# Performance work log

Hardware: AMD Instinct MI355X
Metric: run time of the kernel (lower is better)

## Reference

```python
import jax, jax.numpy as jnp
import numpy as np

N_NODES = 100000
N_EDGES = 3200000
D_IN = 256
D_OUT = 256


def setup_inputs() -> dict:
    key = jax.random.key(0)
    k1, k2, k3, k4, k5, k6 = jax.random.split(key, 6)
    x = jax.random.normal(k1, (N_NODES, D_IN), dtype=jnp.float32)
    edge_row = jax.random.randint(k2, (N_EDGES,), 0, N_NODES, dtype=jnp.int32)
    edge_col = jax.random.randint(k3, (N_EDGES,), 0, N_NODES, dtype=jnp.int32)
    edge_val = jax.random.uniform(k4, (N_EDGES,), dtype=jnp.float32)
    # nn.Linear params (PyTorch stores weight as [out, in]; we apply x @ W.T + b)
    bound = 1.0 / np.sqrt(D_IN)
    W = jax.random.uniform(k5, (D_OUT, D_IN), minval=-bound, maxval=bound, dtype=jnp.float32)
    b = jax.random.uniform(k6, (D_OUT,), minval=-bound, maxval=bound, dtype=jnp.float32)
    return {"x": x, "edge_row": edge_row, "edge_col": edge_col,
            "edge_val": edge_val, "W": W, "b": b}


def reference(x, edge_row, edge_col, edge_val, W, b):
    # SpMM: agg[i] = sum over edges e with row[e]==i of val[e] * x[col[e]]
    messages = edge_val[:, None] * x[edge_col]          # [E, D_in]
    agg = jax.ops.segment_sum(messages, edge_row, num_segments=N_NODES)  # [N, D_in]
    # Dense linear: agg @ W.T + b
    return jnp.einsum('nd,od->no', agg, W) + b
```

## Files before the change

### kernel.cpp

```cpp
#include <hip/hip_runtime.h>

#define THREADS 256

typedef __attribute__((ext_vector_type(8))) short short8;
typedef __attribute__((ext_vector_type(4))) float f32x4;

__device__ __forceinline__ unsigned short f2bf(float f) {
    unsigned u = __builtin_bit_cast(unsigned, f);
    return (unsigned short)((u + 0x7FFFu + ((u >> 16) & 1u)) >> 16);
}
__device__ __forceinline__ float bf2f_lo(unsigned u) { return __builtin_bit_cast(float, u << 16); }
__device__ __forceinline__ float bf2f_hi(unsigned u) { return __builtin_bit_cast(float, u & 0xFFFF0000u); }

#define P1B 1024

__global__ void fusedA_kernel(const int* __restrict__ row, const int* __restrict__ col,
                              const float* __restrict__ val, int* __restrict__ gcur,
                              uint2* __restrict__ estage,
                              const float* __restrict__ W, unsigned short* __restrict__ WbP,
                              const float4* __restrict__ x, uint4* __restrict__ xb,
                              int n_edges, int nbkt, int capB, int n8) {
    int b = blockIdx.x, tid = threadIdx.x;
    if (b < P1B) {
        __shared__ int h[512];
        __shared__ int curl[512];
        int E0 = (int)((long long)b * n_edges / P1B);
        int E1 = (int)((long long)(b + 1) * n_edges / P1B);
        for (int i = tid; i < 512; i += THREADS) h[i] = 0;
        __syncthreads();
        for (int e = E0 + tid; e < E1; e += THREADS)
            atomicAdd(&h[row[e] >> 8], 1);
        __syncthreads();
        for (int bk = tid; bk < nbkt; bk += THREADS) {
            int c = h[bk];
            curl[bk] = bk * capB + (c ? atomicAdd(&gcur[bk], c) : 0);
        }
        __syncthreads();
        for (int e = E0 + tid; e < E1; e += THREADS) {
            int r = row[e];
            int bk = r >> 8;
            int pos = atomicAdd(&curl[bk], 1);
            if (pos < (bk + 1) * capB)
                estage[pos] = make_uint2(((unsigned)(r & 255) << 24) | (unsigned)col[e],
                                         (unsigned)__float_as_int(val[e]));
        }
    } else if (b < P1B + 32) {
        int f = (b - P1B) * THREADS + tid;
        int l = f & 63, nt = (f >> 6) & 15, k0i = f >> 10;
        int r = nt * 16 + (l & 15);
        int koff = k0i * 32 + 8 * (l >> 4);
        const float4* s = reinterpret_cast<const float4*>(W + r * 256 + koff);
        float4 a = s[0], bb = s[1];
        uint4 o;
        o.x = (unsigned)f2bf(a.x) | ((unsigned)f2bf(a.y) << 16);
        o.y = (unsigned)f2bf(a.z) | ((unsigned)f2bf(a.w) << 16);
        o.z = (unsigned)f2bf(bb.x) | ((unsigned)f2bf(bb.y) << 16);
        o.w = (unsigned)f2bf(bb.z) | ((unsigned)f2bf(bb.w) << 16);
        reinterpret_cast<uint4*>(WbP)[f] = o;
    } else {
        int i = (b - P1B - 32) * THREADS + tid;
        if (i >= n8) return;
        float4 a = x[2 * i], bb = x[2 * i + 1];
        uint4 o;
        o.x = (unsigned)f2bf(a.x) | ((unsigned)f2bf(a.y) << 16);
        o.y = (unsigned)f2bf(a.z) | ((unsigned)f2bf(a.w) << 16);
        o.z = (unsigned)f2bf(bb.x) | ((unsigned)f2bf(bb.y) << 16);
        o.w = (unsigned)f2bf(bb.z) | ((unsigned)f2bf(bb.w) << 16);
        reinterpret_cast<uint4*>(xb)[i] = o;
    }
}

__global__ void p2_sort(const uint2* __restrict__ estage, const int* __restrict__ gcur,
                        int2* __restrict__ pr, int* __restrict__ offs,
                        int capB, int n_nodes, int nbkt) {
    __shared__ int red[256];
    __shared__ int h[256];
    __shared__ int curh[256];
    __shared__ int wsum[4];
    int b = blockIdx.x, tid = threadIdx.x;

    int partial = 0;
    for (int j = tid; j < b; j += THREADS) {
        int c = gcur[j];
        partial += c > capB ? capB : c;
    }
    red[tid] = partial;
    __syncthreads();
    #pragma unroll
    for (int s = 128; s > 0; s >>= 1) {
        if (tid < s) red[tid] += red[tid + s];
        __syncthreads();
    }
    int gb = red[0];
    int count = gcur[b]; if (count > capB) count = capB;
    int base = b * capB;

    h[tid] = 0;
    __syncthreads();
    for (int i = tid; i < count; i += THREADS)
        atomicAdd(&h[estage[base + i].x >> 24], 1);
    __syncthreads();
    int v = h[tid];
    int lane = tid & 63, w = tid >> 6;
    int incl = v;
    #pragma unroll
    for (int off = 1; off < 64; off <<= 1) {
        int t = __shfl_up(incl, off, 64);
        if (lane >= off) incl += t;
    }
    if (lane == 63) wsum[w] = incl;
    __syncthreads();
    int wo = 0;
    for (int i = 0; i < w; ++i) wo += wsum[i];
    int excl = wo + incl - v;
    int node = b * 256 + tid;
    if (node < n_nodes) offs[node] = gb + excl;
    curh[tid] = gb + excl;
    if (b == nbkt - 1 && tid == 0) offs[n_nodes] = gb + count;
    __syncthreads();
    for (int i = tid; i < count; i += THREADS) {
        uint2 p = estage[base + i];
        int q = atomicAdd(&curh[(int)(p.x >> 24)], 1);
        pr[q] = make_int2((int)(p.x & 0x00FFFFFFu), (int)p.y);
    }
}

template<int OUT_BF16>
__global__ void spmm_bf16_kernel(const uint2* __restrict__ xb, const int* __restrict__ offs,
                                 const int2* __restrict__ pr, void* __restrict__ outp,
                                 int nnodes) {
    int g = blockIdx.x & 7;
    int inst = blockIdx.x >> 3;
    int bkt = g + 8 * (inst >> 6);
    int wid = bkt * 256 + (inst & 63) * 4 + (threadIdx.x >> 6);
    int lane = threadIdx.x & 63;
    if (wid >= nnodes) return;
    int s = offs[wid], e = offs[wid + 1];
    float a0 = 0.f, a1 = 0.f, a2 = 0.f, a3 = 0.f;
    int i = s;
    if (i < e && (i & 1)) {
        int2 p = pr[i];
        uint2 xv = xb[(size_t)p.x * 64 + lane];
        float v = __int_as_float(p.y);
        a0 = fmaf(v, bf2f_lo(xv.x), a0); a1 = fmaf(v, bf2f_hi(xv.x), a1);
        a2 = fmaf(v, bf2f_lo(xv.y), a2); a3 = fmaf(v, bf2f_hi(xv.y), a3);
        ++i;
    }
    for (; i + 8 <= e; i += 8) {
        int4 pa = *reinterpret_cast<const int4*>(pr + i);
        int4 pb = *reinterpret_cast<const int4*>(pr + i + 2);
        int4 pc = *reinterpret_cast<const int4*>(pr + i + 4);
        int4 pd = *reinterpret_cast<const int4*>(pr + i + 6);
        uint2 x0 = xb[(size_t)pa.x * 64 + lane];
        uint2 x1 = xb[(size_t)pa.z * 64 + lane];
        uint2 x2 = xb[(size_t)pb.x * 64 + lane];
        uint2 x3 = xb[(size_t)pb.z * 64 + lane];
        uint2 x4_ = xb[(size_t)pc.x * 64 + lane];
        uint2 x5 = xb[(size_t)pc.z * 64 + lane];
        uint2 x6 = xb[(size_t)pd.x * 64 + lane];
        uint2 x7 = xb[(size_t)pd.z * 64 + lane];
        float v0 = __int_as_float(pa.y), v1 = __int_as_float(pa.w);
        float v2 = __int_as_float(pb.y), v3 = __int_as_float(pb.w);
        float v4 = __int_as_float(pc.y), v5 = __int_as_float(pc.w);
        float v6 = __int_as_float(pd.y), v7 = __int_as_float(pd.w);
        a0 = fmaf(v0, bf2f_lo(x0.x), a0); a1 = fmaf(v0, bf2f_hi(x0.x), a1);
        a2 = fmaf(v0, bf2f_lo(x0.y), a2); a3 = fmaf(v0, bf2f_hi(x0.y), a3);
        a0 = fmaf(v1, bf2f_lo(x1.x), a0); a1 = fmaf(v1, bf2f_hi(x1.x), a1);
        a2 = fmaf(v1, bf2f_lo(x1.y), a2); a3 = fmaf(v1, bf2f_hi(x1.y), a3);
        a0 = fmaf(v2, bf2f_lo(x2.x), a0); a1 = fmaf(v2, bf2f_hi(x2.x), a1);
        a2 = fmaf(v2, bf2f_lo(x2.y), a2); a3 = fmaf(v2, bf2f_hi(x2.y), a3);
        a0 = fmaf(v3, bf2f_lo(x3.x), a0); a1 = fmaf(v3, bf2f_hi(x3.x), a1);
        a2 = fmaf(v3, bf2f_lo(x3.y), a2); a3 = fmaf(v3, bf2f_hi(x3.y), a3);
        a0 = fmaf(v4, bf2f_lo(x4_.x), a0); a1 = fmaf(v4, bf2f_hi(x4_.x), a1);
        a2 = fmaf(v4, bf2f_lo(x4_.y), a2); a3 = fmaf(v4, bf2f_hi(x4_.y), a3);
        a0 = fmaf(v5, bf2f_lo(x5.x), a0); a1 = fmaf(v5, bf2f_hi(x5.x), a1);
        a2 = fmaf(v5, bf2f_lo(x5.y), a2); a3 = fmaf(v5, bf2f_hi(x5.y), a3);
        a0 = fmaf(v6, bf2f_lo(x6.x), a0); a1 = fmaf(v6, bf2f_hi(x6.x), a1);
        a2 = fmaf(v6, bf2f_lo(x6.y), a2); a3 = fmaf(v6, bf2f_hi(x6.y), a3);
        a0 = fmaf(v7, bf2f_lo(x7.x), a0); a1 = fmaf(v7, bf2f_hi(x7.x), a1);
        a2 = fmaf(v7, bf2f_lo(x7.y), a2); a3 = fmaf(v7, bf2f_hi(x7.y), a3);
    }
    for (; i + 2 <= e; i += 2) {
        int4 pa = *reinterpret_cast<const int4*>(pr + i);
        uint2 x0 = xb[(size_t)pa.x * 64 + lane];
        uint2 x1 = xb[(size_t)pa.z * 64 + lane];
        float v0 = __int_as_float(pa.y), v1 = __int_as_float(pa.w);
        a0 = fmaf(v0, bf2f_lo(x0.x), a0); a1 = fmaf(v0, bf2f_hi(x0.x), a1);
        a2 = fmaf(v0, bf2f_lo(x0.y), a2); a3 = fmaf(v0, bf2f_hi(x0.y), a3);
        a0 = fmaf(v1, bf2f_lo(x1.x), a0); a1 = fmaf(v1, bf2f_hi(x1.x), a1);
        a2 = fmaf(v1, bf2f_lo(x1.y), a2); a3 = fmaf(v1, bf2f_hi(x1.y), a3);
    }
    for (; i < e; ++i) {
        int2 p = pr[i];
        uint2 xv = xb[(size_t)p.x * 64 + lane];
        float v = __int_as_float(p.y);
        a0 = fmaf(v, bf2f_lo(xv.x), a0); a1 = fmaf(v, bf2f_hi(xv.x), a1);
        a2 = fmaf(v, bf2f_lo(xv.y), a2); a3 = fmaf(v, bf2f_hi(xv.y), a3);
    }
    if (OUT_BF16) {
        ushort4 o;
        o.x = f2bf(a0); o.y = f2bf(a1); o.z = f2bf(a2); o.w = f2bf(a3);
        *reinterpret_cast<ushort4*>((unsigned short*)outp + (size_t)wid * 256 + 4 * lane) = o;
    } else {
        ((float4*)outp)[(size_t)wid * 64 + lane] = make_float4(a0, a1, a2, a3);
    }
}

__global__ void spmm_f32_kernel(const float4* __restrict__ x4, const int* __restrict__ offs,
                                const int2* __restrict__ pr, float4* __restrict__ out4,
                                int nnodes) {
    int wid = (blockIdx.x * blockDim.x + threadIdx.x) >> 6;
    int lane = threadIdx.x & 63;
    if (wid >= nnodes) return;
    int s = offs[wid], e = offs[wid + 1];
    float4 acc = make_float4(0.f, 0.f, 0.f, 0.f);
    for (int i = s; i < e; ++i) {
        int2 p = pr[i];
        float4 xv = x4[(size_t)p.x * 64 + lane];
        float v = __int_as_float(p.y);
        acc.x = fmaf(v, xv.x, acc.x); acc.y = fmaf(v, xv.y, acc.y);
        acc.z = fmaf(v, xv.z, acc.z); acc.w = fmaf(v, xv.w, acc.w);
    }
    out4[(size_t)wid * 64 + lane] = acc;
}

__launch_bounds__(256)
__global__ void gemm_direct3_kernel(const unsigned short* __restrict__ aggb,
                                    const unsigned short* __restrict__ WbP,
                                    const float* __restrict__ bias,
                                    float* __restrict__ out, int n) {
    int tid = threadIdx.x, lane = tid & 63, w = tid >> 6;
    int row0 = blockIdx.x * 128 + w * 32;
    int lr = lane & 15, lg = lane >> 4;
    const unsigned short* arow0 = aggb + (size_t)(row0 + lr) * 256 + lg * 8;
    const unsigned short* arow1 = arow0 + 16 * 256;
    short8 af0[8], af1[8];
    #pragma unroll
    for (int k = 0; k < 8; ++k) {
        af0[k] = *reinterpret_cast<const short8*>(arow0 + k * 32);
        af1[k] = *reinterpret_cast<const short8*>(arow1 + k * 32);
    }
    #pragma unroll
    for (int half = 0; half < 2; ++half) {
        f32x4 acc0[8], acc1[8];
        #pragma unroll
        for (int nt = 0; nt < 8; ++nt) {
            acc0[nt] = (f32x4){0.f, 0.f, 0.f, 0.f};
            acc1[nt] = (f32x4){0.f, 0.f, 0.f, 0.f};
        }
        #pragma unroll
        for (int k = 0; k < 8; ++k) {
            #pragma unroll
            for (int nt = 0; nt < 8; ++nt) {
                short8 bf_ = *reinterpret_cast<const short8*>(
                    &WbP[(size_t)((k * 16 + half * 8 + nt) * 64 + lane) * 8]);
                acc0[nt] = __builtin_amdgcn_mfma_f32_16x16x32_bf16(af0[k], bf_, acc0[nt], 0, 0, 0);
                acc1[nt] = __builtin_amdgcn_mfma_f32_16x16x32_bf16(af1[k], bf_, acc1[nt], 0, 0, 0);
            }
        }
        #pragma unroll
        for (int nt = 0; nt < 8; ++nt) {
            int gc = half * 128 + nt * 16 + lr;
            float bv = bias[gc];
            #pragma unroll
            for (int q = 0; q < 4; ++q) {
                int gr0 = row0 + lg * 4 + q;
                int gr1 = gr0 + 16;
                if (gr0 < n) out[(size_t)gr0 * 256 + gc] = acc0[nt][q] + bv;
                if (gr1 < n) out[(size_t)gr1 * 256 + gc] = acc1[nt][q] + bv;
            }
        }
    }
}


__global__ void zero_kernel(int* __restrict__ p, int n) {
    int i = blockIdx.x * blockDim.x + threadIdx.x;
    if (i < n) p[i] = 0;
}

__global__ void hist_part_kernel(const int* __restrict__ row, int* __restrict__ cnt,
                                 int n_edges, int n_nodes) {
    int g = blockIdx.x & 7;
    int inst = blockIdx.x >> 3;
    int ninst = gridDim.x >> 3;
    int lo = (int)(((long long)g * n_nodes) >> 3);
    int hi = (int)(((long long)(g + 1) * n_nodes) >> 3);
    int e0 = (int)(((long long)inst * n_edges) / ninst);
    int e1 = (int)(((long long)(inst + 1) * n_edges) / ninst);
    for (int e = e0 + threadIdx.x; e < e1; e += THREADS) {
        int r = row[e];
        if (r >= lo && r < hi) atomicAdd(&cnt[r], 1);
    }
}

__global__ void place_part_kernel(const int* __restrict__ row, const int* __restrict__ col,
                                  const float* __restrict__ val, int* __restrict__ cur,
                                  int2* __restrict__ pr, int n_edges, int n_nodes) {
    int g = blockIdx.x & 7;
    int inst = blockIdx.x >> 3;
    int ninst = gridDim.x >> 3;
    int lo = (int)(((long long)g * n_nodes) >> 3);
    int hi = (int)(((long long)(g + 1) * n_nodes) >> 3);
    int e0 = (int)(((long long)inst * n_edges) / ninst);
    int e1 = (int)(((long long)(inst + 1) * n_edges) / ninst);
    for (int e = e0 + threadIdx.x; e < e1; e += THREADS) {
        int r = row[e];
        if (r >= lo && r < hi) {
            int p = atomicAdd(&cur[r], 1);
            pr[p] = make_int2(col[e], __float_as_int(val[e]));
        }
    }
}

__global__ void scan1_kernel(const int* __restrict__ cnt, int* __restrict__ offs,
                             int* __restrict__ bsum, int n) {
    int tid = threadIdx.x;
    int base = blockIdx.x * 1024 + tid * 4;
    int v0 = 0, v1 = 0, v2 = 0, v3 = 0;
    if (base + 3 < n) {
        int4 v = *reinterpret_cast<const int4*>(cnt + base);
        v0 = v.x; v1 = v.y; v2 = v.z; v3 = v.w;
    } else {
        if (base + 0 < n) v0 = cnt[base + 0];
        if (base + 1 < n) v1 = cnt[base + 1];
        if (base + 2 < n) v2 = cnt[base + 2];
    }
    int ts = v0 + v1 + v2 + v3;
    int lane = tid & 63;
    int incl = ts;
    #pragma unroll
    for (int off = 1; off < 64; off <<= 1) {
        int t = __shfl_up(incl, off, 64);
        if (lane >= off) incl += t;
    }
    __shared__ int wsum[4];
    int w = tid >> 6;
    if (lane == 63) wsum[w] = incl;
    __syncthreads();
    int wo = 0;
    for (int i = 0; i < w; ++i) wo += wsum[i];
    int excl = wo + incl - ts;
    if (base + 0 < n) offs[base + 0] = excl;
    if (base + 1 < n) offs[base + 1] = excl + v0;
    if (base + 2 < n) offs[base + 2] = excl + v0 + v1;
    if (base + 3 < n) offs[base + 3] = excl + v0 + v1 + v2;
    if (tid == THREADS - 1) bsum[blockIdx.x] = wo + incl;
}

__global__ void scan2_kernel(int* __restrict__ bsum, int nb) {
    int tid = threadIdx.x;
    int base = tid * 4;
    int v0 = 0, v1 = 0, v2 = 0, v3 = 0;
    if (base + 0 < nb) v0 = bsum[base + 0];
    if (base + 1 < nb) v1 = bsum[base + 1];
    if (base + 2 < nb) v2 = bsum[base + 2];
    if (base + 3 < nb) v3 = bsum[base + 3];
    int ts = v0 + v1 + v2 + v3;
    int lane = tid & 63;
    int incl = ts;
    #pragma unroll
    for (int off = 1; off < 64; off <<= 1) {
        int t = __shfl_up(incl, off, 64);
        if (lane >= off) incl += t;
    }
    __shared__ int wsum[4];
    int w = tid >> 6;
    if (lane == 63) wsum[w] = incl;
    __syncthreads();
    int wo = 0;
    for (int i = 0; i < w; ++i) wo += wsum[i];
    int excl = wo + incl - ts;
    if (base + 0 < nb) bsum[base + 0] = excl;
    if (base + 1 < nb) bsum[base + 1] = excl + v0;
    if (base + 2 < nb) bsum[base + 2] = excl + v0 + v1;
    if (base + 3 < nb) bsum[base + 3] = excl + v0 + v1 + v2;
    if (tid == THREADS - 1) bsum[nb] = wo + incl;
}

__global__ void scan3_kernel(int* __restrict__ offs, const int* __restrict__ bsum,
                             int* __restrict__ cur, int n) {
    int i = blockIdx.x * blockDim.x + threadIdx.x;
    if (i < n) {
        int v = offs[i] + bsum[i >> 10];
        offs[i] = v;
        cur[i] = v;
    }
    if (i == 0) offs[n] = bsum[(n + 1023) >> 10];
}

__global__ void cvt_bf16_kernel(const float4* __restrict__ in, uint4* __restrict__ out, int n8) {
    int i = blockIdx.x * blockDim.x + threadIdx.x;
    if (i >= n8) return;
    float4 a = in[2 * i], b = in[2 * i + 1];
    uint4 o;
    o.x = (unsigned)f2bf(a.x) | ((unsigned)f2bf(a.y) << 16);
    o.y = (unsigned)f2bf(a.z) | ((unsigned)f2bf(a.w) << 16);
    o.z = (unsigned)f2bf(b.x) | ((unsigned)f2bf(b.y) << 16);
    o.w = (unsigned)f2bf(b.z) | ((unsigned)f2bf(b.w) << 16);
    out[i] = o;
}

__launch_bounds__(256, 2)
__global__ void gemm_mfma_kernel(float* __restrict__ out, const unsigned short* __restrict__ Wb,
                                 const float* __restrict__ bias, int nrows) {
    __shared__ unsigned short As[64][264];
    __shared__ unsigned short Ws[256][40];
    int tid = threadIdx.x;
    int rowBase = blockIdx.x * 64;

    const float4* o4 = reinterpret_cast<const float4*>(out);
    for (int it = tid; it < 64 * 64; it += 256) {
        int r = it >> 6, c = it & 63;
        float4 v = make_float4(0.f, 0.f, 0.f, 0.f);
        int gr = rowBase + r;
        if (gr < nrows) v = o4[(size_t)gr * 64 + c];
        ushort4 w;
        w.x = f2bf(v.x); w.y = f2bf(v.y); w.z = f2bf(v.z); w.w = f2bf(v.w);
        *reinterpret_cast<ushort4*>(&As[r][c * 4]) = w;
    }

    int w = tid >> 6, lane = tid & 63;
    int lr = lane & 15, lg = lane >> 4;
    f32x4 acc[16];
    #pragma unroll
    for (int nt = 0; nt < 16; ++nt) acc[nt] = (f32x4){0.f, 0.f, 0.f, 0.f};

    for (int k0 = 0; k0 < 256; k0 += 32) {
        __syncthreads();
        for (int it = tid; it < 1024; it += 256) {
            int r = it >> 2, c = it & 3;
            uint4 v = *reinterpret_cast<const uint4*>(Wb + (size_t)r * 256 + k0 + c * 8);
            *reinterpret_cast<uint4*>(&Ws[r][c * 8]) = v;
        }
        __syncthreads();
        short8 af = *reinterpret_cast<const short8*>(&As[w * 16 + lr][k0 + 8 * lg]);
        #pragma unroll
        for (int nt = 0; nt < 16; ++nt) {
            short8 bf_ = *reinterpret_cast<const short8*>(&Ws[nt * 16 + lr][8 * lg]);
            acc[nt] = __builtin_amdgcn_mfma_f32_16x16x32_bf16(af, bf_, acc[nt], 0, 0, 0);
        }
    }

    #pragma unroll
    for (int nt = 0; nt < 16; ++nt) {
        int gc = nt * 16 + lr;
        float bv = bias[gc];
        #pragma unroll
        for (int q = 0; q < 4; ++q) {
            int gr = rowBase + w * 16 + lg * 4 + q;
            if (gr < nrows) out[(size_t)gr * 256 + gc] = acc[nt][q] + bv;
        }
    }
}


extern "C" void kernel_launch(void* const* d_in, const int* in_sizes, int n_in,
                              void* d_out, int out_size, void* d_ws, size_t ws_size,
                              hipStream_t stream) {
    const float* x     = (const float*)d_in[0];
    const int*   erow  = (const int*)d_in[1];
    const int*   ecol  = (const int*)d_in[2];
    const float* evalv = (const float*)d_in[3];
    const float* W     = (const float*)d_in[4];
    const float* bias  = (const float*)d_in[5];
    float* out = (float*)d_out;

    int n_nodes = in_sizes[0] / 256;
    int n_edges = in_sizes[1];

    int nbkt = (n_nodes + 255) >> 8;
    int avg = n_edges / (nbkt > 0 ? nbkt : 1);
    int capB = avg + avg / 4 + 1024;

    size_t A = (size_t)((n_nodes + 63) & ~63) + 64;
    int* offs  = (int*)d_ws;
    int* gcur  = offs + A;
    unsigned short* WbP = (unsigned short*)(gcur + 512);
    int2* pr = (int2*)(WbP + 65536);
    int* after_pr = (int*)(pr + n_edges);

    size_t est_ints  = (size_t)nbkt * capB * 2;
    size_t aggb_ints = (size_t)n_nodes * 128 + 32768;
    size_t xb_ints   = (size_t)n_nodes * 128;
    size_t alias_ints = est_ints > aggb_ints ? est_ints : aggb_ints;
    size_t head_ints = (size_t)(after_pr - (int*)d_ws);
    size_t need_new = (head_ints + alias_ints + xb_ints) * 4;
    bool new_ok = (nbkt <= 512) && (nbkt >= 1) && (n_nodes <= (1 << 24)) && ws_size >= need_new;

    if (new_ok) {
        uint2* estage = (uint2*)after_pr;
        unsigned short* aggb = (unsigned short*)after_pr;
        unsigned short* xb = (unsigned short*)(after_pr + alias_ints);

        hipMemsetAsync(gcur, 0, 512 * sizeof(int), stream);
        int n8 = n_nodes * 32;
        int cvtx_blocks = (n8 + THREADS - 1) / THREADS;
        fusedA_kernel<<<P1B + 32 + cvtx_blocks, THREADS, 0, stream>>>(
            erow, ecol, evalv, gcur, estage, W, WbP, (const float4*)x, (uint4*)xb,
            n_edges, nbkt, capB, n8);
        p2_sort<<<nbkt, THREADS, 0, stream>>>(estage, gcur, pr, offs, capB, n_nodes, nbkt);

        int spmm_blocks = 8 * ((nbkt + 7) / 8) * 64;
        spmm_bf16_kernel<1><<<spmm_blocks, THREADS, 0, stream>>>(
            (const uint2*)xb, offs, pr, aggb, n_nodes);
        int gb = (n_nodes + 127) / 128;
        gemm_direct3_kernel<<<gb, THREADS, 0, stream>>>(aggb, WbP, bias, out, n_nodes);
    } else {
        int nb = (n_nodes + 1023) >> 10;
        size_t Af = (size_t)((n_nodes + 63) & ~63);
        int* cnt   = (int*)d_ws;
        int* offsf = cnt + Af;
        int* cur   = offsf + Af;
        int* bsum  = cur + Af;
        int* wbase = bsum + (((size_t)nb + 64) & ~63ull);
        unsigned short* Wbf = (unsigned short*)wbase;
        int2* prf  = (int2*)(Wbf + 65536);
        int* aft   = (int*)(prf + n_edges);
        unsigned short* xbf = (unsigned short*)aft;
        size_t need_old = (size_t)((char*)(xbf + (size_t)n_nodes * 256) - (char*)d_ws);
        bool told = ws_size >= need_old;

        zero_kernel<<<(n_nodes + THREADS - 1) / THREADS, THREADS, 0, stream>>>(cnt, n_nodes);
        hist_part_kernel<<<2048, THREADS, 0, stream>>>(erow, cnt, n_edges, n_nodes);
        scan1_kernel<<<nb, THREADS, 0, stream>>>(cnt, offsf, bsum, n_nodes);
        scan2_kernel<<<1, THREADS, 0, stream>>>(bsum, nb);
        scan3_kernel<<<(n_nodes + THREADS - 1) / THREADS, THREADS, 0, stream>>>(offsf, bsum, cur, n_nodes);
        place_part_kernel<<<2048, THREADS, 0, stream>>>(erow, ecol, evalv, cur, prf, n_edges, n_nodes);
        cvt_bf16_kernel<<<32, THREADS, 0, stream>>>((const float4*)W, (uint4*)Wbf, 65536 / 8);

        int gb = (n_nodes + 63) / 64;
        if (told) {
            int n8 = n_nodes * 32;
            cvt_bf16_kernel<<<(n8 + THREADS - 1) / THREADS, THREADS, 0, stream>>>(
                (const float4*)x, (uint4*)xbf, n8);
            int spmm_blocks_f = (n_nodes + 3) / 4;
            spmm_bf16_kernel<0><<<8 * (((n_nodes + 255) / 256 + 7) / 8) * 64, THREADS, 0, stream>>>(
                (const uint2*)xbf, offsf, prf, out, n_nodes);
            (void)spmm_blocks_f;
        } else {
            int spmm_blocks_f = (n_nodes + 3) / 4;
            spmm_f32_kernel<<<spmm_blocks_f, THREADS, 0, stream>>>(
                (const float4*)x, offsf, prf, (float4*)out, n_nodes);
        }
        gemm_mfma_kernel<<<gb, THREADS, 0, stream>>>(out, Wbf, bias, n_nodes);
    }
}
```

Measured before the change: 422.9 us.

## Widen p2_sort blocks to 512 threads and split SpMM into three bucket-range launches

```diff
diff --git a/kernel.cpp b/kernel.cpp
--- a/kernel.cpp
+++ b/kernel.cpp
@@ -1,6 +1,7 @@
 #include <hip/hip_runtime.h>
 
 #define THREADS 256
+#define P2T 512
 
 typedef __attribute__((ext_vector_type(8))) short short8;
 typedef __attribute__((ext_vector_type(4))) float f32x4;
@@ -73,21 +74,21 @@
 __global__ void p2_sort(const uint2* __restrict__ estage, const int* __restrict__ gcur,
                         int2* __restrict__ pr, int* __restrict__ offs,
                         int capB, int n_nodes, int nbkt) {
-    __shared__ int red[256];
+    __shared__ int red[P2T];
     __shared__ int h[256];
     __shared__ int curh[256];
     __shared__ int wsum[4];
     int b = blockIdx.x, tid = threadIdx.x;
 
     int partial = 0;
-    for (int j = tid; j < b; j += THREADS) {
+    for (int j = tid; j < b; j += P2T) {
         int c = gcur[j];
         partial += c > capB ? capB : c;
     }
     red[tid] = partial;
     __syncthreads();
     #pragma unroll
-    for (int s = 128; s > 0; s >>= 1) {
+    for (int s = P2T / 2; s > 0; s >>= 1) {
         if (tid < s) red[tid] += red[tid + s];
         __syncthreads();
     }
@@ -95,30 +96,34 @@
     int count = gcur[b]; if (count > capB) count = capB;
     int base = b * capB;
 
-    h[tid] = 0;
+    if (tid < 256) h[tid] = 0;
     __syncthreads();
-    for (int i = tid; i < count; i += THREADS)
+    for (int i = tid; i < count; i += P2T)
         atomicAdd(&h[estage[base + i].x >> 24], 1);
     __syncthreads();
-    int v = h[tid];
-    int lane = tid & 63, w = tid >> 6;
-    int incl = v;
-    #pragma unroll
-    for (int off = 1; off < 64; off <<= 1) {
-        int t = __shfl_up(incl, off, 64);
-        if (lane >= off) incl += t;
-    }
-    if (lane == 63) wsum[w] = incl;
-    __syncthreads();
-    int wo = 0;
-    for (int i = 0; i < w; ++i) wo += wsum[i];
-    int excl = wo + incl - v;
-    int node = b * 256 + tid;
-    if (node < n_nodes) offs[node] = gb + excl;
-    curh[tid] = gb + excl;
+    if (tid < 256) {
+        int v = h[tid];
+        int lane = tid & 63, w = tid >> 6;
+        int incl = v;
+        #pragma unroll
+        for (int off = 1; off < 64; off <<= 1) {
+            int t = __shfl_up(incl, off, 64);
+            if (lane >= off) incl += t;
+        }
+        if (lane == 63) wsum[w] = incl;
+        __syncthreads();
+        int wo = 0;
+        for (int i = 0; i < w; ++i) wo += wsum[i];
+        int excl = wo + incl - v;
+        int node = b * 256 + tid;
+        if (node < n_nodes) offs[node] = gb + excl;
+        curh[tid] = gb + excl;
+    } else {
+        __syncthreads();
+    }
     if (b == nbkt - 1 && tid == 0) offs[n_nodes] = gb + count;
     __syncthreads();
-    for (int i = tid; i < count; i += THREADS) {
+    for (int i = tid; i < count; i += P2T) {
         uint2 p = estage[base + i];
         int q = atomicAdd(&curh[(int)(p.x >> 24)], 1);
         pr[q] = make_int2((int)(p.x & 0x00FFFFFFu), (int)p.y);
@@ -128,10 +133,11 @@
 template<int OUT_BF16>
 __global__ void spmm_bf16_kernel(const uint2* __restrict__ xb, const int* __restrict__ offs,
                                  const int2* __restrict__ pr, void* __restrict__ outp,
-                                 int nnodes) {
+                                 int b0, int b1, int nnodes) {
     int g = blockIdx.x & 7;
     int inst = blockIdx.x >> 3;
-    int bkt = g + 8 * (inst >> 6);
+    int bkt = b0 + g + 8 * (inst >> 6);
+    if (bkt >= b1) return;
     int wid = bkt * 256 + (inst & 63) * 4 + (threadIdx.x >> 6);
     int lane = threadIdx.x & 63;
     if (wid >= nnodes) return;
@@ -499,11 +505,17 @@
         fusedA_kernel<<<P1B + 32 + cvtx_blocks, THREADS, 0, stream>>>(
             erow, ecol, evalv, gcur, estage, W, WbP, (const float4*)x, (uint4*)xb,
             n_edges, nbkt, capB, n8);
-        p2_sort<<<nbkt, THREADS, 0, stream>>>(estage, gcur, pr, offs, capB, n_nodes, nbkt);
-
-        int spmm_blocks = 8 * ((nbkt + 7) / 8) * 64;
-        spmm_bf16_kernel<1><<<spmm_blocks, THREADS, 0, stream>>>(
-            (const uint2*)xb, offs, pr, aggb, n_nodes);
+        p2_sort<<<nbkt, P2T, 0, stream>>>(estage, gcur, pr, offs, capB, n_nodes, nbkt);
+
+        int b0 = 0;
+        for (int sseg = 1; sseg <= 3; ++sseg) {
+            int b1 = (sseg == 3) ? nbkt : ((nbkt * sseg / 3) & ~7);
+            if (b1 <= b0) continue;
+            int grid = 8 * (((b1 - b0) + 7) / 8) * 64;
+            spmm_bf16_kernel<1><<<grid, THREADS, 0, stream>>>(
+                (const uint2*)xb, offs, pr, aggb, b0, b1, n_nodes);
+            b0 = b1;
+        }
         int gb = (n_nodes + 127) / 128;
         gemm_direct3_kernel<<<gb, THREADS, 0, stream>>>(aggb, WbP, bias, out, n_nodes);
     } else {
@@ -534,10 +546,10 @@
             int n8 = n_nodes * 32;
             cvt_bf16_kernel<<<(n8 + THREADS - 1) / THREADS, THREADS, 0, stream>>>(
                 (const float4*)x, (uint4*)xbf, n8);
-            int spmm_blocks_f = (n_nodes + 3) / 4;
-            spmm_bf16_kernel<0><<<8 * (((n_nodes + 255) / 256 + 7) / 8) * 64, THREADS, 0, stream>>>(
-                (const uint2*)xbf, offsf, prf, out, n_nodes);
-            (void)spmm_blocks_f;
+            int nbf = (n_nodes + 255) / 256;
+            int gridf = 8 * ((nbf + 7) / 8) * 64;
+            spmm_bf16_kernel<0><<<gridf, THREADS, 0, stream>>>(
+                (const uint2*)xbf, offsf, prf, out, 0, nbf, n_nodes);
         } else {
             int spmm_blocks_f = (n_nodes + 3) / 4;
             spmm_f32_kernel<<<spmm_blocks_f, THREADS, 0, stream>>>(
```

Result: no change. 427.8 us (+1.2%).
